# Performance work log

Hardware: AMD Instinct MI355X
Metric: run time of the kernel (lower is better)

Reference implementation:

```python
import jax, jax.numpy as jnp
import numpy as np
import itertools, math

M_MODES = 10
N_PHOT = 5
IN_MODES = np.array([0, 2, 4, 6, 8])  # input_state = [1,0,1,0,...], 5 photons
INV_SQRT2 = 0.7071067811865476

# Fock output bases (lexicographic ordering)
ROWS_NB = np.array(list(itertools.combinations(range(M_MODES), N_PHOT)), np.int32)          # [252,5] no-bunching
ROWS_B = np.array(list(itertools.combinations_with_replacement(range(M_MODES), N_PHOT)), np.int32)  # [2002,5] bunched

def _norms(rows):
    out = []
    for r in rows:
        c = np.bincount(r, minlength=M_MODES)
        out.append(float(np.prod([math.factorial(int(v)) for v in c])))
    return np.array(out, np.float32)

NORM_NB = _norms(ROWS_NB)  # all ones
NORM_B = _norms(ROWS_B)

# Glynn sign vectors for n=5 permanents (delta_0 fixed to +1): [16,5]
_D = np.array(list(itertools.product([1.0, -1.0], repeat=N_PHOT - 1)), np.float32)
DELTAS = np.concatenate([np.ones((_D.shape[0], 1), np.float32), _D], axis=1)
DSIGNS = np.prod(DELTAS, axis=1)


def _mzi(t1, t2):
    # BS // PS(t1) // BS // PS(t2); BS = (1/sqrt2)[[1,i],[i,1]], PS on first mode of pair
    B = jnp.array([[1.0, 1.0j], [1.0j, 1.0]], dtype=jnp.complex64) * INV_SQRT2
    e1 = jnp.exp(1j * t1)
    e2 = jnp.exp(1j * t2)
    M1 = B * jnp.stack([e1, jnp.ones_like(e1)])[:, None]   # PS(t1) @ BS
    M2 = B @ M1                                            # BS @ ...
    return M2 * jnp.stack([e2, jnp.ones_like(e2)])[:, None]  # PS(t2) @ ...


def interferometer(phases):
    """Rectangular (Clements) mesh on 10 modes with 45 MZIs; phases [45,2] -> U [10,10] complex."""
    Ts = jax.vmap(lambda p: _mzi(p[0], p[1]))(phases)  # [45,2,2]
    U = jnp.eye(M_MODES, dtype=jnp.complex64)
    k = 0
    for layer in range(M_MODES):
        for p in range(layer % 2, M_MODES - 1, 2):
            U = U.at[p:p + 2, :].set(Ts[k] @ U[p:p + 2, :])
            k += 1
    return U


def batched_permanent(Ms):
    """Glynn formula for [...,5,5] complex matrices."""
    D = jnp.asarray(DELTAS, dtype=Ms.dtype)       # [16,5]
    s = jnp.asarray(DSIGNS, dtype=Ms.dtype)       # [16]
    rowsum = jnp.einsum('di,...ij->...dj', D, Ms)  # [...,16,5]
    return jnp.einsum('d,...d->...', s, jnp.prod(rowsum, axis=-1)) / (2 ** (N_PHOT - 1))


def fock_probs(U, rows, norm):
    """U [B,10,10]; rows [K,5] output-mode indices (with repetition for bunching); norm [K]."""
    M = U[:, rows][..., IN_MODES]        # [B,K,5,5]
    perm = batched_permanent(M)          # [B,K]
    return (jnp.abs(perm) ** 2) / jnp.asarray(norm)


def _forward(x, W_down, b_down, phases_l1, phases_r1, phases_lf, phases_rf, W_out, b_out):
    h = (x @ W_down + b_down) / jnp.pi                 # downscale + DivideByPi -> [B,10]
    WL1 = interferometer(phases_l1)
    WR1 = interferometer(phases_r1)
    U1 = jnp.einsum('mk,bk,kn->bmn', WR1, jnp.exp(1j * h), WL1)  # WR @ diag(e^{i phi}) @ WL
    e1 = fock_probs(U1, ROWS_NB, NORM_NB)              # [B,252], no_bunching=True
    # final circuit: 252 px phase shifters round-robin over 10 modes -> phases add per mode
    Bsz = e1.shape[0]
    pad = jnp.pad(e1, ((0, 0), (0, 260 - 252)))
    phi2 = pad.reshape(Bsz, 26, M_MODES).sum(axis=1)   # [B,10]
    WLF = interferometer(phases_lf)
    WRF = interferometer(phases_rf)
    UF = jnp.einsum('mk,bk,kn->bmn', WRF, jnp.exp(1j * phi2), WLF)
    probs = fock_probs(UF, ROWS_B, NORM_B)             # [B,2002], bunched Fock states
    return probs @ W_out + b_out                       # [B,num_classes]


def setup_inputs() -> dict:
    key = jax.random.key(0)
    ks = jax.random.split(key, 9)
    two_pi = 2.0 * np.pi
    return {
        'x': jax.random.normal(ks[0], (128, 784), dtype=jnp.float32),
        'W_down': jax.random.normal(ks[1], (784, 10), dtype=jnp.float32) * 0.05,
        'b_down': jax.random.normal(ks[2], (10,), dtype=jnp.float32) * 0.05,
        'phases_l1': jax.random.uniform(ks[3], (45, 2), dtype=jnp.float32) * two_pi,
        'phases_r1': jax.random.uniform(ks[4], (45, 2), dtype=jnp.float32) * two_pi,
        'phases_lf': jax.random.uniform(ks[5], (45, 2), dtype=jnp.float32) * two_pi,
        'phases_rf': jax.random.uniform(ks[6], (45, 2), dtype=jnp.float32) * two_pi,
        'W_out': jax.random.normal(ks[7], (2002, 10), dtype=jnp.float32) * 0.02,
        'b_out': jax.random.normal(ks[8], (10,), dtype=jnp.float32) * 0.02,
    }


def reference(x, W_down, b_down, phases_l1, phases_r1, phases_lf, phases_rf, W_out, b_out):
    return _forward(x, W_down, b_down, phases_l1, phases_r1, phases_lf, phases_rf, W_out, b_out)
```

## Files before the change

kernel.cpp:

```cpp
#include <hip/hip_runtime.h>
#include <math.h>


#define PI_F 3.14159265358979323846f

__device__ __forceinline__ float2 cmul(float2 a, float2 b) {
  return make_float2(fmaf(a.x, b.x, -a.y * b.y), fmaf(a.x, b.y, a.y * b.x));
}
__device__ __forceinline__ float2 cadd(float2 a, float2 b) {
  return make_float2(a.x + b.x, a.y + b.y);
}
__device__ __forceinline__ float2 cscale(float2 a, float s) {
  return make_float2(a.x * s, a.y * s);
}
__device__ __forceinline__ float2 imul(float2 a) {
  return make_float2(-a.y, a.x);
}

__device__ __forceinline__ void unrank5f(int rank, float cnt0, float m0,
                                         int c[5]) {
  float r = (float)rank;
  float cnt = cnt0, m = m0, j = 4.f;
  int x = 0;
#pragma unroll
  for (int i = 0; i < 5; i++) {
    while (r >= cnt) {
      r -= cnt;
      cnt = cnt * (m - j) / m;
      m -= 1.f;
      x++;
    }
    c[i] = x;
    cnt = cnt * j / m;
    m -= 1.f;
    j -= 1.f;
    x++;
  }
}

__device__ __forceinline__ float2 prod5(const float2 rs[5]) {
  return cmul(cmul(cmul(rs[0], rs[1]), cmul(rs[2], rs[3])), rs[4]);
}

__device__ __forceinline__ float2 perm5(const float2 M[5][5]) {
  float2 rs[5];
#pragma unroll
  for (int j = 0; j < 5; j++) {
    rs[j] = M[0][j];
#pragma unroll
    for (int i = 1; i < 5; i++) rs[j] = cadd(rs[j], M[i][j]);
  }
  float2 acc = prod5(rs);
#pragma unroll
  for (int t = 1; t < 16; t++) {
    const int g = t ^ (t >> 1);
    const int bit = (t & 1) ? 0 : ((t & 2) ? 1 : ((t & 4) ? 2 : 3));
    const int i = bit + 1;
    const float step = ((g >> bit) & 1) ? -2.0f : 2.0f;
#pragma unroll
    for (int j = 0; j < 5; j++) {
      rs[j].x = fmaf(step, M[i][j].x, rs[j].x);
      rs[j].y = fmaf(step, M[i][j].y, rs[j].y);
    }
    float2 p = prod5(rs);
    const float s = (__popc(g) & 1) ? -1.0f : 1.0f;
    acc.x = fmaf(s, p.x, acc.x);
    acc.y = fmaf(s, p.y, acc.y);
  }
  return make_float2(acc.x * (1.0f / 16.0f), acc.y * (1.0f / 16.0f));
}

__global__ __launch_bounds__(256) void k_prefix(
    const float* __restrict__ x, const float* __restrict__ Wd,
    const float* __restrict__ bd, const float* __restrict__ ph_l1,
    const float* __restrict__ ph_r1, const float* __restrict__ ph_lf,
    const float* __restrict__ ph_rf, const float* __restrict__ bout,
    float2* __restrict__ UFws, float* __restrict__ out) {
  const int b = blockIdx.x, tid = threadIdx.x;

  __shared__ float2 T[4][45][4];
  __shared__ float2 Ui[4][100];
  __shared__ float2 Ub[100];
  __shared__ float  e1s[252];
  __shared__ float  red[4][10];
  __shared__ float2 v[10];

  float hacc[10];
#pragma unroll
  for (int c = 0; c < 10; c++) hacc[c] = 0.f;
  for (int i = tid; i < 784; i += 256) {
    float xv = x[b * 784 + i];
    const float* w = Wd + i * 10;
#pragma unroll
    for (int c = 0; c < 10; c++) hacc[c] = fmaf(xv, w[c], hacc[c]);
  }

  if (tid < 180) {
    const int which = tid / 45, m = tid % 45;
    const float* ph = (which == 0) ? ph_l1
                    : (which == 1) ? ph_r1
                    : (which == 2) ? ph_lf : ph_rf;
    float t1 = ph[m * 2 + 0], t2 = ph[m * 2 + 1];
    float s1, c1, s2, c2;
    __sincosf(t1, &s1, &c1);
    __sincosf(t2, &s2, &c2);
    float2 e2  = make_float2(c2, s2);
    float2 e1m = make_float2(c1 - 1.f, s1);
    float2 e1p = make_float2(c1 + 1.f, s1);
    T[which][m][0] = cscale(cmul(e2, e1m), 0.5f);
    T[which][m][1] = cscale(cmul(e2, imul(e1p)), 0.5f);
    T[which][m][2] = cscale(imul(e1p), 0.5f);
    T[which][m][3] = make_float2(0.5f * (1.f - c1), -0.5f * s1);
  }

  {
    const int lane = tid & 63, wave = tid >> 6;
#pragma unroll
    for (int c = 0; c < 10; c++) {
      float r = hacc[c];
#pragma unroll
      for (int d = 32; d > 0; d >>= 1) r += __shfl_down(r, d);
      if (lane == 0) red[wave][c] = r;
    }
  }
  __syncthreads();

  if (tid < 40) {
    const int which = tid / 10, n = tid % 10;
    float2 u[10];
#pragma unroll
    for (int m = 0; m < 10; m++)
      u[m] = make_float2(m == n ? 1.f : 0.f, 0.f);
    int kb = 0;
#pragma unroll
    for (int layer = 0; layer < 10; layer++) {
      const int start = layer & 1;
      const int npairs = 5 - start;
#pragma unroll
      for (int pi = 0; pi < 5; pi++) {
        if (pi < npairs) {
          const int p = start + 2 * pi;
          const int k = kb + pi;
          float2 u0 = u[p], u1 = u[p + 1];
          u[p]     = cadd(cmul(T[which][k][0], u0), cmul(T[which][k][1], u1));
          u[p + 1] = cadd(cmul(T[which][k][2], u0), cmul(T[which][k][3], u1));
        }
      }
      kb += npairs;
    }
#pragma unroll
    for (int m = 0; m < 10; m++) Ui[which][m * 10 + n] = u[m];
  } else if (tid >= 64 && tid < 74) {
    const int c = tid - 64;
    float s = red[0][c] + red[1][c] + red[2][c] + red[3][c] + bd[c];
    s *= (1.0f / PI_F);
    float sn, cs;
    __sincosf(s, &sn, &cs);
    v[c] = make_float2(cs, sn);
  }
  __syncthreads();

  if (tid < 100) {
    const int m = tid / 10, n = tid % 10;
    float2 acc = make_float2(0.f, 0.f);
#pragma unroll
    for (int k = 0; k < 10; k++)
      acc = cadd(acc, cmul(cmul(Ui[1][m * 10 + k], v[k]), Ui[0][k * 10 + n]));
    Ub[tid] = acc;
  }
  __syncthreads();

  if (tid < 252) {
    int c[5];
    unrank5f(tid, 126.f, 9.f, c);
    float2 M[5][5];
#pragma unroll
    for (int i = 0; i < 5; i++)
#pragma unroll
      for (int j = 0; j < 5; j++) M[i][j] = Ub[c[i] * 10 + 2 * j];
    float2 p = perm5(M);
    e1s[tid] = p.x * p.x + p.y * p.y;
  }
  __syncthreads();

  if (tid < 10) {
    float s = 0.f;
    for (int idx = tid; idx < 252; idx += 10) s += e1s[idx];
    float sn, cs;
    __sincosf(s, &sn, &cs);
    v[tid] = make_float2(cs, sn);
  }
  __syncthreads();

  if (tid < 100) {
    const int m = tid / 10, n = tid % 10;
    float2 acc = make_float2(0.f, 0.f);
#pragma unroll
    for (int k = 0; k < 10; k++)
      acc = cadd(acc, cmul(cmul(Ui[3][m * 10 + k], v[k]), Ui[2][k * 10 + n]));
    UFws[b * 100 + tid] = acc;
  }
  if (tid < 10) out[b * 10 + tid] = bout[tid];
}

__global__ __launch_bounds__(256) void k_perms(const float2* __restrict__ UFws,
                                               const float* __restrict__ Wout,
                                               float* __restrict__ out) {
  const int b = blockIdx.x >> 3, chunk = blockIdx.x & 7;
  const int tid = threadIdx.x;
  const int k = chunk * 256 + tid;
  __shared__ float2 U[100];
  __shared__ float red[4][10];
  if (tid < 50)
    ((float4*)U)[tid] = ((const float4*)(UFws + b * 100))[tid];
  __syncthreads();

  float acc[10];
#pragma unroll
  for (int c = 0; c < 10; c++) acc[c] = 0.f;

  if (k < 2002) {
    int c5[5];
    unrank5f(k, 715.f, 13.f, c5);
    int modes[5];
#pragma unroll
    for (int i = 0; i < 5; i++) modes[i] = c5[i] - i;
    float2 M[5][5];
#pragma unroll
    for (int i = 0; i < 5; i++)
#pragma unroll
      for (int j = 0; j < 5; j++) M[i][j] = U[modes[i] * 10 + 2 * j];
    float2 p = perm5(M);
    float norm = 1.f, cnt = 1.f;
#pragma unroll
    for (int i = 1; i < 5; i++) {
      cnt = (modes[i] == modes[i - 1]) ? cnt + 1.f : 1.f;
      norm *= cnt;
    }
    const float pv = (p.x * p.x + p.y * p.y) / norm;
    const float2* w2 = (const float2*)Wout + k * 5;
#pragma unroll
    for (int c = 0; c < 5; c++) {
      float2 w = w2[c];
      acc[2 * c + 0] = pv * w.x;
      acc[2 * c + 1] = pv * w.y;
    }
  }

  const int lane = tid & 63, wave = tid >> 6;
#pragma unroll
  for (int c = 0; c < 10; c++) {
    float r = acc[c];
#pragma unroll
    for (int d = 32; d > 0; d >>= 1) r += __shfl_down(r, d);
    if (lane == 0) red[wave][c] = r;
  }
  __syncthreads();
  if (tid < 10) {
    float s = red[0][tid] + red[1][tid] + red[2][tid] + red[3][tid];
    atomicAdd(&out[b * 10 + tid], s);
  }
}

extern "C" void kernel_launch(void* const* d_in, const int* in_sizes, int n_in,
                              void* d_out, int out_size, void* d_ws,
                              size_t ws_size, hipStream_t stream) {
  const float* x    = (const float*)d_in[0];
  const float* Wd   = (const float*)d_in[1];
  const float* bd   = (const float*)d_in[2];
  const float* pl1  = (const float*)d_in[3];
  const float* pr1  = (const float*)d_in[4];
  const float* plf  = (const float*)d_in[5];
  const float* prf  = (const float*)d_in[6];
  const float* Wout = (const float*)d_in[7];
  const float* bout = (const float*)d_in[8];
  float* out = (float*)d_out;

  float2* UFws = (float2*)d_ws;

  k_prefix<<<128, 256, 0, stream>>>(x, Wd, bd, pl1, pr1, plf, prf, bout, UFws,
                                    out);
  k_perms<<<1024, 256, 0, stream>>>(UFws, Wout, out);
}
```

Before: 90.25 us.

## Fuse prefix and bunched-permanent kernels into a single per-sample kernel

Merges the prefix kernel and the bunched-permanent kernel so each block computes its unitary, then loops over all 2002 output states itself and writes the final logits directly. This removes the second launch, the global workspace round trip and the atomic accumulation. In exchange, the permanent stage runs on only 128 blocks, each doing 8 serial iterations, which leaves many CUs idle.

```diff
diff --git a/kernel.cpp b/kernel.cpp
--- a/kernel.cpp
+++ b/kernel.cpp
@@ -70,12 +70,12 @@
   return make_float2(acc.x * (1.0f / 16.0f), acc.y * (1.0f / 16.0f));
 }
 
-__global__ __launch_bounds__(256) void k_prefix(
+__global__ __launch_bounds__(256) void k_all(
     const float* __restrict__ x, const float* __restrict__ Wd,
     const float* __restrict__ bd, const float* __restrict__ ph_l1,
     const float* __restrict__ ph_r1, const float* __restrict__ ph_lf,
-    const float* __restrict__ ph_rf, const float* __restrict__ bout,
-    float2* __restrict__ UFws, float* __restrict__ out) {
+    const float* __restrict__ ph_rf, const float* __restrict__ Wout,
+    const float* __restrict__ bout, float* __restrict__ out) {
   const int b = blockIdx.x, tid = threadIdx.x;
 
   __shared__ float2 T[4][45][4];
@@ -198,67 +198,59 @@
 #pragma unroll
     for (int k = 0; k < 10; k++)
       acc = cadd(acc, cmul(cmul(Ui[3][m * 10 + k], v[k]), Ui[2][k * 10 + n]));
-    UFws[b * 100 + tid] = acc;
-  }
-  if (tid < 10) out[b * 10 + tid] = bout[tid];
-}
-
-__global__ __launch_bounds__(256) void k_perms(const float2* __restrict__ UFws,
-                                               const float* __restrict__ Wout,
-                                               float* __restrict__ out) {
-  const int b = blockIdx.x >> 3, chunk = blockIdx.x & 7;
-  const int tid = threadIdx.x;
-  const int k = chunk * 256 + tid;
-  __shared__ float2 U[100];
-  __shared__ float red[4][10];
-  if (tid < 50)
-    ((float4*)U)[tid] = ((const float4*)(UFws + b * 100))[tid];
+    Ub[tid] = acc;
+  }
   __syncthreads();
 
   float acc[10];
 #pragma unroll
   for (int c = 0; c < 10; c++) acc[c] = 0.f;
-
-  if (k < 2002) {
-    int c5[5];
-    unrank5f(k, 715.f, 13.f, c5);
-    int modes[5];
-#pragma unroll
-    for (int i = 0; i < 5; i++) modes[i] = c5[i] - i;
-    float2 M[5][5];
-#pragma unroll
-    for (int i = 0; i < 5; i++)
-#pragma unroll
-      for (int j = 0; j < 5; j++) M[i][j] = U[modes[i] * 10 + 2 * j];
-    float2 p = perm5(M);
-    float norm = 1.f, cnt = 1.f;
-#pragma unroll
-    for (int i = 1; i < 5; i++) {
-      cnt = (modes[i] == modes[i - 1]) ? cnt + 1.f : 1.f;
-      norm *= cnt;
-    }
-    const float pv = (p.x * p.x + p.y * p.y) / norm;
-    const float2* w2 = (const float2*)Wout + k * 5;
-#pragma unroll
-    for (int c = 0; c < 5; c++) {
-      float2 w = w2[c];
-      acc[2 * c + 0] = pv * w.x;
-      acc[2 * c + 1] = pv * w.y;
-    }
-  }
-
-  const int lane = tid & 63, wave = tid >> 6;
-#pragma unroll
-  for (int c = 0; c < 10; c++) {
-    float r = acc[c];
-#pragma unroll
-    for (int d = 32; d > 0; d >>= 1) r += __shfl_down(r, d);
-    if (lane == 0) red[wave][c] = r;
+#pragma unroll
+  for (int it = 0; it < 8; it++) {
+    const int k = tid + it * 256;
+    if (k < 2002) {
+      int c5[5];
+      unrank5f(k, 715.f, 13.f, c5);
+      int modes[5];
+#pragma unroll
+      for (int i = 0; i < 5; i++) modes[i] = c5[i] - i;
+      float2 M[5][5];
+#pragma unroll
+      for (int i = 0; i < 5; i++)
+#pragma unroll
+        for (int j = 0; j < 5; j++) M[i][j] = Ub[modes[i] * 10 + 2 * j];
+      float2 p = perm5(M);
+      float norm = 1.f, cnt = 1.f;
+#pragma unroll
+      for (int i = 1; i < 5; i++) {
+        cnt = (modes[i] == modes[i - 1]) ? cnt + 1.f : 1.f;
+        norm *= cnt;
+      }
+      const float pv = (p.x * p.x + p.y * p.y) / norm;
+      const float2* w2 = (const float2*)Wout + k * 5;
+#pragma unroll
+      for (int c = 0; c < 5; c++) {
+        float2 w = w2[c];
+        acc[2 * c + 0] = fmaf(pv, w.x, acc[2 * c + 0]);
+        acc[2 * c + 1] = fmaf(pv, w.y, acc[2 * c + 1]);
+      }
+    }
+  }
+
+  {
+    const int lane = tid & 63, wave = tid >> 6;
+#pragma unroll
+    for (int c = 0; c < 10; c++) {
+      float r = acc[c];
+#pragma unroll
+      for (int d = 32; d > 0; d >>= 1) r += __shfl_down(r, d);
+      if (lane == 0) red[wave][c] = r;
+    }
   }
   __syncthreads();
   if (tid < 10) {
     float s = red[0][tid] + red[1][tid] + red[2][tid] + red[3][tid];
-    atomicAdd(&out[b * 10 + tid], s);
+    out[b * 10 + tid] = s + bout[tid];
   }
 }
 
@@ -276,9 +268,6 @@
   const float* bout = (const float*)d_in[8];
   float* out = (float*)d_out;
 
-  float2* UFws = (float2*)d_ws;
-
-  k_prefix<<<128, 256, 0, stream>>>(x, Wd, bd, pl1, pr1, plf, prf, bout, UFws,
-                                    out);
-  k_perms<<<1024, 256, 0, stream>>>(UFws, Wout, out);
-}
+  k_all<<<128, 256, 0, stream>>>(x, Wd, bd, pl1, pr1, plf, prf, Wout, bout,
+                                 out);
+}
```

Result: slower. 100.3 us (+11.2%).

## Merge prefix phases into wave-specialized paths, removing a block barrier

Applied to the files above, without the earlier changes.

The k_prefix front end is restructured so wave 0 computes the MZI transfer matrices and then immediately builds the interferometer unitaries, while wave 2 alone computes the downsampling dot products with float4 loads and a wave-level xor-shuffle reduction. This removes one __syncthreads and the cross-wave shared-memory reduction of the earlier layout. The cost is that the 180 sincos/T computations now run on only 40 threads (up to 5 each), and the 784x10 matvec runs on one wave instead of four, which lengthens per-thread serial work. The overall effect depends on whether the saved barrier outweighs the added serial work.

```diff
diff --git a/kernel.cpp b/kernel.cpp
--- a/kernel.cpp
+++ b/kernel.cpp
@@ -82,81 +82,90 @@
   __shared__ float2 Ui[4][100];
   __shared__ float2 Ub[100];
   __shared__ float  e1s[252];
-  __shared__ float  red[4][10];
   __shared__ float2 v[10];
 
-  float hacc[10];
-#pragma unroll
-  for (int c = 0; c < 10; c++) hacc[c] = 0.f;
-  for (int i = tid; i < 784; i += 256) {
-    float xv = x[b * 784 + i];
-    const float* w = Wd + i * 10;
-#pragma unroll
-    for (int c = 0; c < 10; c++) hacc[c] = fmaf(xv, w[c], hacc[c]);
-  }
-
-  if (tid < 180) {
-    const int which = tid / 45, m = tid % 45;
-    const float* ph = (which == 0) ? ph_l1
-                    : (which == 1) ? ph_r1
-                    : (which == 2) ? ph_lf : ph_rf;
-    float t1 = ph[m * 2 + 0], t2 = ph[m * 2 + 1];
-    float s1, c1, s2, c2;
-    __sincosf(t1, &s1, &c1);
-    __sincosf(t2, &s2, &c2);
-    float2 e2  = make_float2(c2, s2);
-    float2 e1m = make_float2(c1 - 1.f, s1);
-    float2 e1p = make_float2(c1 + 1.f, s1);
-    T[which][m][0] = cscale(cmul(e2, e1m), 0.5f);
-    T[which][m][1] = cscale(cmul(e2, imul(e1p)), 0.5f);
-    T[which][m][2] = cscale(imul(e1p), 0.5f);
-    T[which][m][3] = make_float2(0.5f * (1.f - c1), -0.5f * s1);
-  }
-
-  {
-    const int lane = tid & 63, wave = tid >> 6;
-#pragma unroll
-    for (int c = 0; c < 10; c++) {
-      float r = hacc[c];
-#pragma unroll
-      for (int d = 32; d > 0; d >>= 1) r += __shfl_down(r, d);
-      if (lane == 0) red[wave][c] = r;
-    }
-  }
-  __syncthreads();
-
-  if (tid < 40) {
-    const int which = tid / 10, n = tid % 10;
-    float2 u[10];
-#pragma unroll
-    for (int m = 0; m < 10; m++)
-      u[m] = make_float2(m == n ? 1.f : 0.f, 0.f);
-    int kb = 0;
-#pragma unroll
-    for (int layer = 0; layer < 10; layer++) {
-      const int start = layer & 1;
-      const int npairs = 5 - start;
-#pragma unroll
-      for (int pi = 0; pi < 5; pi++) {
-        if (pi < npairs) {
-          const int p = start + 2 * pi;
-          const int k = kb + pi;
-          float2 u0 = u[p], u1 = u[p + 1];
-          u[p]     = cadd(cmul(T[which][k][0], u0), cmul(T[which][k][1], u1));
-          u[p + 1] = cadd(cmul(T[which][k][2], u0), cmul(T[which][k][3], u1));
+  if (tid < 64) {
+    if (tid < 40) {
+      const int which = tid / 10, n = tid % 10;
+      const float* ph = (which == 0) ? ph_l1
+                      : (which == 1) ? ph_r1
+                      : (which == 2) ? ph_lf : ph_rf;
+#pragma unroll
+      for (int t5 = 0; t5 < 5; t5++) {
+        const int m = n + 10 * t5;
+        if (m < 45) {
+          float t1 = ph[m * 2 + 0], t2 = ph[m * 2 + 1];
+          float s1, c1, s2, c2;
+          __sincosf(t1, &s1, &c1);
+          __sincosf(t2, &s2, &c2);
+          float2 e2  = make_float2(c2, s2);
+          float2 e1m = make_float2(c1 - 1.f, s1);
+          float2 e1p = make_float2(c1 + 1.f, s1);
+          T[which][m][0] = cscale(cmul(e2, e1m), 0.5f);
+          T[which][m][1] = cscale(cmul(e2, imul(e1p)), 0.5f);
+          T[which][m][2] = cscale(imul(e1p), 0.5f);
+          T[which][m][3] = make_float2(0.5f * (1.f - c1), -0.5f * s1);
         }
       }
-      kb += npairs;
-    }
-#pragma unroll
-    for (int m = 0; m < 10; m++) Ui[which][m * 10 + n] = u[m];
-  } else if (tid >= 64 && tid < 74) {
-    const int c = tid - 64;
-    float s = red[0][c] + red[1][c] + red[2][c] + red[3][c] + bd[c];
-    s *= (1.0f / PI_F);
-    float sn, cs;
-    __sincosf(s, &sn, &cs);
-    v[c] = make_float2(cs, sn);
+      float2 u[10];
+#pragma unroll
+      for (int m = 0; m < 10; m++)
+        u[m] = make_float2(m == n ? 1.f : 0.f, 0.f);
+      int kb = 0;
+#pragma unroll
+      for (int layer = 0; layer < 10; layer++) {
+        const int start = layer & 1;
+        const int npairs = 5 - start;
+#pragma unroll
+        for (int pi = 0; pi < 5; pi++) {
+          if (pi < npairs) {
+            const int p = start + 2 * pi;
+            const int k = kb + pi;
+            float2 u0 = u[p], u1 = u[p + 1];
+            u[p]     = cadd(cmul(T[which][k][0], u0), cmul(T[which][k][1], u1));
+            u[p + 1] = cadd(cmul(T[which][k][2], u0), cmul(T[which][k][3], u1));
+          }
+        }
+        kb += npairs;
+      }
+#pragma unroll
+      for (int m = 0; m < 10; m++) Ui[which][m * 10 + n] = u[m];
+    }
+  } else if (tid >= 128 && tid < 192) {
+    const int lane = tid - 128;
+    float acc[10];
+#pragma unroll
+    for (int c = 0; c < 10; c++) acc[c] = 0.f;
+    const float4* x4 = (const float4*)(x + b * 784);
+#pragma unroll
+    for (int it = 0; it < 4; it++) {
+      const int q = lane + it * 64;
+      if (q < 196) {
+        float4 xv = x4[q];
+        const float4* w4 = (const float4*)(Wd + 40 * q);
+        float W[40];
+#pragma unroll
+        for (int j = 0; j < 10; j++) {
+          float4 wv = w4[j];
+          W[4 * j + 0] = wv.x; W[4 * j + 1] = wv.y;
+          W[4 * j + 2] = wv.z; W[4 * j + 3] = wv.w;
+        }
+        const float xe[4] = {xv.x, xv.y, xv.z, xv.w};
+#pragma unroll
+        for (int s = 0; s < 40; s++)
+          acc[s % 10] = fmaf(xe[s / 10], W[s], acc[s % 10]);
+      }
+    }
+#pragma unroll
+    for (int d = 32; d > 0; d >>= 1)
+#pragma unroll
+      for (int c = 0; c < 10; c++) acc[c] += __shfl_xor(acc[c], d);
+    if (lane < 10) {
+      float s = (acc[lane] + bd[lane]) * (1.0f / PI_F);
+      float sn, cs;
+      __sincosf(s, &sn, &cs);
+      v[lane] = make_float2(cs, sn);
+    }
   }
   __syncthreads();
 
```

New measurement: 85.87 us. -4.9%, faster.
